# Kernel tuning notes

Hardware: AMD Instinct MI355X
Metric: run time of the kernel (lower is better)

## Reference

```python
import jax, jax.numpy as jnp
import numpy as np

B, S, D, NL = 512, 200, 128, 2
N_ITEMS = 50001
DH = 2 * D
DFF = 4 * D


def layer_norm(x, g, b, eps=1e-5):
    mu = x.mean(-1, keepdims=True)
    v = ((x - mu) ** 2).mean(-1, keepdims=True)
    return (x - mu) / jnp.sqrt(v + eps) * g + b


def lru_scan(h, lamb0, mask):
    # h: (B, L, DH) complex64, lamb0: (DH,) complex64, mask: (B, L) bool
    Bb, L, Dh = h.shape
    log2_L = int(np.ceil(np.log2(L)))
    lamb = lamb0.reshape(1, Dh)
    for i in range(1, log2_L + 1):
        l = 2 ** i
        h = h.reshape(Bb * L // l, l, Dh)
        m = mask.reshape(Bb * L // l, l)
        h1, h2 = h[:, : l // 2], h[:, l // 2:]
        if i > 1:
            lamb = jnp.concatenate([lamb, lamb * lamb[-1]], axis=0)  # powers lambda^1..lambda^(l/2)
        carry_gate = m[:, l // 2 - 1 : l // 2, None].astype(h.dtype)
        h2 = h2 + lamb * h1[:, -1:] * carry_gate
        h = jnp.concatenate([h1, h2], axis=1)
    return h.reshape(Bb, L, Dh)


def _forward(token_emb, emb_ln_g, emb_ln_b, params_log,
             in_wr, in_wi, in_br, in_bi, out_wr, out_wi, out_br, out_bi,
             lru_ln_g, lru_ln_b, w1, b1, w2, b2, ffn_ln_g, ffn_ln_b,
             item_seq, item_seq_len):
    mask = item_seq > 0                      # (B, S)
    x = token_emb[item_seq]                  # (B, S, D)
    x = layer_norm(x, emb_ln_g, emb_ln_b)
    seq_len = item_seq.shape[1]
    L = 2 ** int(np.ceil(np.log2(seq_len)))
    pad = L - seq_len
    x = jnp.pad(x, ((0, 0), (pad, 0), (0, 0)))        # left-pad seq to power of 2
    m = jnp.pad(mask, ((0, 0), (pad, 0)))
    n_layers = params_log.shape[0]
    for li in range(n_layers):
        pl = jnp.exp(params_log[li])                  # (3, DH): nu, theta, gamma
        nu, theta, gamma = pl[0], pl[1], pl[2]
        lamb0 = jnp.exp(jax.lax.complex(-nu, theta))  # (DH,)
        in_w = jax.lax.complex(in_wr[li], in_wi[li])
        in_b = jax.lax.complex(in_br[li], in_bi[li])
        h = (jnp.einsum('bld,hd->blh', x.astype(jnp.complex64), in_w) + in_b) * gamma
        h = lru_scan(h, lamb0, m)
        out_w = jax.lax.complex(out_wr[li], out_wi[li])
        out_b = jax.lax.complex(out_br[li], out_bi[li])
        y = (jnp.einsum('blh,dh->bld', h, out_w) + out_b).real + x
        x = layer_norm(y, lru_ln_g[li], lru_ln_b[li])
        # positionwise FFN with residual + post-LN
        hff = jax.nn.gelu(jnp.einsum('bld,fd->blf', x, w1[li]) + b1[li], approximate=False)
        x = layer_norm(jnp.einsum('blf,df->bld', hff, w2[li]) + b2[li] + x,
                       ffn_ln_g[li], ffn_ln_b[li])
    x = x[:, -seq_len:]                               # (B, S, D)
    idx = item_seq_len - 1
    return x[jnp.arange(x.shape[0]), idx]             # (B, D)


def setup_inputs() -> dict:
    key = jax.random.key(0)
    ks = jax.random.split(key, 24)
    std = 0.02
    item_seq = jax.random.randint(ks[0], (B, S), 0, N_ITEMS)
    item_seq_len = jax.random.randint(ks[1], (B,), 1, S + 1)
    # LRU diagonal init (matches torch init)
    r_min, r_max = 0.8, 0.99
    u1 = jax.random.uniform(ks[2], (NL, DH))
    u2 = jax.random.uniform(ks[3], (NL, DH))
    nu_log = jnp.log(-0.5 * jnp.log(u1 * (r_max ** 2 - r_min ** 2) + r_min ** 2))
    theta_log = jnp.log(u2 * 2.0 * np.pi)
    gamma_log = 0.5 * jnp.log(1.0 - jnp.exp(-2.0 * jnp.exp(nu_log)))
    params_log = jnp.stack([nu_log, theta_log, gamma_log], axis=1)  # (NL, 3, DH)
    rn = lambda k, sh: jax.random.normal(k, sh, dtype=jnp.float32) * std
    return {
        'token_emb': rn(ks[4], (N_ITEMS, D)),
        'emb_ln_g': jnp.ones((D,), jnp.float32), 'emb_ln_b': jnp.zeros((D,), jnp.float32),
        'params_log': params_log,
        'in_wr': rn(ks[5], (NL, DH, D)), 'in_wi': rn(ks[6], (NL, DH, D)),
        'in_br': rn(ks[7], (NL, DH)), 'in_bi': rn(ks[8], (NL, DH)),
        'out_wr': rn(ks[9], (NL, D, DH)), 'out_wi': rn(ks[10], (NL, D, DH)),
        'out_br': rn(ks[11], (NL, D)), 'out_bi': rn(ks[12], (NL, D)),
        'lru_ln_g': jnp.ones((NL, D), jnp.float32), 'lru_ln_b': jnp.zeros((NL, D), jnp.float32),
        'w1': rn(ks[13], (NL, DFF, D)), 'b1': rn(ks[14], (NL, DFF)),
        'w2': rn(ks[15], (NL, D, DFF)), 'b2': rn(ks[16], (NL, D)),
        'ffn_ln_g': jnp.ones((NL, D), jnp.float32), 'ffn_ln_b': jnp.zeros((NL, D), jnp.float32),
        'item_seq': item_seq, 'item_seq_len': item_seq_len,
    }


def reference(token_emb, emb_ln_g, emb_ln_b, params_log,
              in_wr, in_wi, in_br, in_bi, out_wr, out_wi, out_br, out_bi,
              lru_ln_g, lru_ln_b, w1, b1, w2, b2, ffn_ln_g, ffn_ln_b,
              item_seq, item_seq_len):
    return _forward(token_emb, emb_ln_g, emb_ln_b, params_log,
                    in_wr, in_wi, in_br, in_bi, out_wr, out_wi, out_br, out_bi,
                    lru_ln_g, lru_ln_b, w1, b1, w2, b2, ffn_ln_g, ffn_ln_b,
                    item_seq, item_seq_len)
```

## Files before the change

kernel.cpp:

```cpp
#include <hip/hip_runtime.h>
#include <hip/hip_bf16.h>
#include <math.h>

#define B_TOT 512
#define SEQ   200
#define D     128
#define DH    256
#define DFF   512
#define LPAD  256
#define PADL  56
#define NLAY  2
#define CST   260

typedef __attribute__((ext_vector_type(8))) short bf16x8;
typedef __attribute__((ext_vector_type(4))) float floatx4;

static __device__ inline float bf2f(ushort u) {
    union { unsigned int i; float f; } v; v.i = ((unsigned int)u) << 16; return v.f;
}
static __device__ inline ushort f2bf(float x) {
    union { float f; unsigned int i; } v; v.f = x;
    unsigned int r = (v.i + 0x7FFFu + ((v.i >> 16) & 1u)) >> 16;
    return (ushort)r;
}
static __device__ inline unsigned int pkbf(float a, float b) {
    union { __hip_bfloat162 h; unsigned int u; } v;
    v.h = __float22bfloat162_rn(make_float2(a, b));
    return v.u;
}
static __device__ inline void gld_lds16(const void* g, void* l) {
    __builtin_amdgcn_global_load_lds(
        (const __attribute__((address_space(1))) unsigned int*)g,
        (__attribute__((address_space(3))) unsigned int*)l, 16, 0, 0);
}

static __device__ inline size_t haddr(int b, int s, int k) {
    int p  = k >> 8;
    int ch = k & 255;
    int g  = ch >> 5;
    int cl = ch & 31;
    return (((((size_t)b * 8 + g) * 2 + p) * SEQ + s) * 32 + cl);
}

__global__ void setup_all_kernel(const float* __restrict__ params_log,
                                 const float* __restrict__ in_br,
                                 const float* __restrict__ in_bi,
                                 const float* __restrict__ in_wr,
                                 const float* __restrict__ in_wi,
                                 const float* __restrict__ out_wr,
                                 const float* __restrict__ out_wi,
                                 const float* __restrict__ w1,
                                 const float* __restrict__ w2,
                                 ushort* __restrict__ Winb,
                                 ushort* __restrict__ W2effb,
                                 ushort* __restrict__ w1b,
                                 ushort* __restrict__ w2b,
                                 float* __restrict__ lam_pow,
                                 float* __restrict__ scale_in,
                                 float* __restrict__ bias_in)
{
    int idx = blockIdx.x * blockDim.x + threadIdx.x;
    int li = idx >> 16;
    int e  = idx & 65535;

    {
        int gp = e >> 12, rem = e & 4095;
        int q = rem >> 3, e8 = rem & 7;
        int r = q >> 4, cs = q & 15;
        int c16 = cs ^ (r & 7);
        int n = (r < 16) ? (gp * 16 + r) : (256 + gp * 16 + (r - 16));
        int d = c16 * 8 + e8;
        float wv = (n < DH) ? in_wr[((size_t)li * DH + n) * D + d]
                            : in_wi[((size_t)li * DH + (n - DH)) * D + d];
        Winb[idx] = f2bf(wv);
    }
    {
        int k0c = e >> 13, rem = e & 8191;
        int q = rem >> 3, e8 = rem & 7;
        int r = q >> 3, cs = q & 7;
        int c16 = cs ^ (r & 7);
        int k = k0c * 64 + c16 * 8 + e8;
        float w2v = (k < DH) ? out_wr[((size_t)li * D + r) * DH + k]
                             : -out_wi[((size_t)li * D + r) * DH + (k - DH)];
        W2effb[idx] = f2bf(w2v);
    }
    {
        int row = e >> 7, col = e & 127;
        int ffc = row >> 7, rl = row & 127;
        int c16 = col >> 3, e8 = col & 7;
        int cs = c16 ^ (rl & 7);
        w1b[li * 65536 + ffc * 16384 + rl * 128 + cs * 8 + e8] = f2bf(w1[idx]);
    }
    {
        int dd2 = e >> 9, kk = e & 511;
        int ffc = kk >> 7, klc = kk & 127;
        int c16 = klc >> 3, e8 = klc & 7;
        int cs = c16 ^ (dd2 & 7);
        w2b[li * 65536 + ffc * 16384 + dd2 * 128 + cs * 8 + e8] = f2bf(w2[idx]);
    }

    if (blockIdx.x < NLAY) {
        int pli = blockIdx.x;
        int c = threadIdx.x;
        const float* pl = params_log + (size_t)pli * 3 * DH;
        float nu = expf(pl[c]);
        float th = expf(pl[DH + c]);
        float ga = expf(pl[2 * DH + c]);
        float mag = expf(-nu);
        float lr = mag * cosf(th);
        float lim = mag * sinf(th);
        float2* lp = (float2*)(lam_pow + (size_t)pli * 65536) + (size_t)c * 128;
        float pr = lr, pi = lim;
        lp[0] = make_float2(pr, pi);
        for (int k = 1; k < 128; ++k) {
            float nr = pr * lr - pi * lim;
            float ni = pr * lim + pi * lr;
            pr = nr; pi = ni;
            lp[k] = make_float2(pr, pi);
        }
        scale_in[pli * 2 * DH + c]      = ga;
        scale_in[pli * 2 * DH + DH + c] = ga;
        bias_in[pli * 2 * DH + c]       = in_br[pli * DH + c] * ga;
        bias_in[pli * 2 * DH + DH + c]  = in_bi[pli * DH + c] * ga;
    }
}

__global__ __launch_bounds__(512) void build_rowmap_kernel(
    const int* __restrict__ lenp, int Bc,
    int* __restrict__ total, int* __restrict__ rowmap)
{
    __shared__ int pre[513];
    int tid = threadIdx.x;
    int lv = (tid < Bc) ? lenp[tid] : 0;
    pre[tid + 1] = lv;
    if (tid == 0) pre[0] = 0;
    __syncthreads();
    for (int ofs = 1; ofs < 512; ofs <<= 1) {
        int v = pre[tid + 1];
        int vv = (tid + 1 > ofs) ? pre[tid + 1 - ofs] : 0;
        __syncthreads();
        pre[tid + 1] = v + vv;
        __syncthreads();
    }
    if (tid == 0) total[0] = pre[Bc];
    if (tid < Bc) {
        int base = pre[tid];
        int n = lv;
        int rb = tid * SEQ;
        for (int s = 0; s < n; ++s) rowmap[base + s] = rb + s;
    }
}

__global__ __launch_bounds__(256) void embed_ln_kernel(
    const float* __restrict__ emb, const int* __restrict__ seq,
    const int* __restrict__ lenp,
    const float* __restrict__ g, const float* __restrict__ bt,
    ushort* __restrict__ x)
{
    int row  = blockIdx.x * 4 + (threadIdx.x >> 6);
    int lane = threadIdx.x & 63;
    int b = row / SEQ, s = row - b * SEQ;
    if (s >= lenp[b]) return;
    int item = seq[row];
    float2 v = *(const float2*)(emb + (size_t)item * D + lane * 2);
    float ssum = v.x + v.y;
#pragma unroll
    for (int o = 32; o > 0; o >>= 1) ssum += __shfl_xor(ssum, o);
    float mu = ssum * (1.0f / D);
    float d0 = v.x - mu, d1 = v.y - mu;
    float vs = d0 * d0 + d1 * d1;
#pragma unroll
    for (int o = 32; o > 0; o >>= 1) vs += __shfl_xor(vs, o);
    float rstd = rsqrtf(vs * (1.0f / D) + 1e-5f);
    float2 gg = *(const float2*)(g + lane * 2);
    float2 bb = *(const float2*)(bt + lane * 2);
    unsigned int o2 = pkbf(d0 * rstd * gg.x + bb.x, d1 * rstd * gg.y + bb.y);
    *(unsigned int*)(x + (size_t)row * D + lane * 2) = o2;
}

template <bool LAST>
__global__ __launch_bounds__(512) void inproj_scan_kernel(
    const ushort* __restrict__ X, const ushort* __restrict__ Win,
    ushort* __restrict__ H, const float2* __restrict__ lamT,
    const int* __restrict__ seq, const int* __restrict__ lenp,
    const float* __restrict__ scale_in, const float* __restrict__ bias_in)
{
    __shared__ __align__(16) char smem[36864];
    __shared__ __align__(16) float mkf[LPAD];
    char*  Wsm = smem;
    char*  xs  = smem + 8192;
    float* stR = (float*)smem;
    float* stI = stR + 16 * CST;

    int gp = blockIdx.x, b = blockIdx.y;
    int tid = threadIdx.x;
    int l = tid & 63, w = tid >> 6;
    int ct = w & 1;
    int rq = w >> 1;
    int lr = l & 15, lq = l >> 4;
    int wbase = tid & ~63;

    int c  = tid >> 5;
    int tl = tid & 31;
    int t0 = tl * 8;
    int lbase = l & 32;

    int s_b = lenp[b] - 1;
    int tile_max = s_b >> 4;
    int nrows = (tile_max + 1) * 16;
    int tb = s_b + PADL;
    bool activeT = (t0 <= tb);

    const ushort* xrow = X + (size_t)b * SEQ * 128;
    gld_lds16(Win + (size_t)gp * 4096 + (size_t)tid * 8,
              Wsm + (size_t)wbase * 16);
    int nrA = nrows < 112 ? nrows : 112;
#pragma unroll
    for (int it = 0; it < 4; ++it) {
        int rbase = it * 32 + w * 4;
        int r = rbase + lq;
        int cs = lr ^ (r & 7);
        if (r < nrA)
            gld_lds16(xrow + (size_t)r * 128 + cs * 8, xs + rbase * 256);
    }

    const float2* myl = lamT + (size_t)(gp * 16 + c) * 128;

    if (tid < LPAD) {
        int t = tid;
        float m = 0.f;
        if (t >= PADL) m = (seq[(size_t)b * SEQ + (t - PADL)] > 0) ? 1.f : 0.f;
        mkf[t] = m;
    }
    __syncthreads();

    bf16x8 wf[4];
#pragma unroll
    for (int kk = 0; kk < 4; ++kk) {
        int ca = kk * 4 + lq;
        int wr = ct * 16 + lr;
        wf[kk] = *(const bf16x8*)(Wsm + wr * 256 + ((ca ^ (wr & 7)) * 16));
    }
    int tstart = rq ? (3 * rq + 1) : 0;
    int tcnt   = rq ? 3 : 4;
    floatx4 acc[4];
#pragma unroll
    for (int tt = 0; tt < 4; ++tt) acc[tt] = (floatx4)0.f;

    if (rq < 2) {
#pragma unroll
        for (int tt = 0; tt < 4; ++tt) {
            if (tt < tcnt && (tstart + tt) <= tile_max) {
                int t  = tstart + tt;
                int ar = t * 16 + lr;
#pragma unroll
                for (int kk = 0; kk < 4; ++kk) {
                    int ca = kk * 4 + lq;
                    bf16x8 af = *(const bf16x8*)(xs + ar * 256 + ((ca ^ (ar & 7)) * 16));
                    acc[tt] = __builtin_amdgcn_mfma_f32_16x16x32_bf16(wf[kk], af, acc[tt], 0, 0, 0);
                }
            }
        }
    }
    __syncthreads();

    if (nrows > 112) {
        int nrB = nrows < 200 ? nrows : 200;
#pragma unroll
        for (int it = 0; it < 3; ++it) {
            int rbase = it * 32 + w * 4;
            int rl_ = rbase + lq;
            int gr = 112 + rl_;
            int cs = lr ^ (rl_ & 7);
            if (gr < nrB)
                gld_lds16(xrow + (size_t)gr * 128 + cs * 8, xs + rbase * 256);
        }
    }
    __syncthreads();

    if (rq >= 2) {
#pragma unroll
        for (int tt = 0; tt < 4; ++tt) {
            if (tt < tcnt && (tstart + tt) <= tile_max) {
                int t  = tstart + tt;
                int ar = (t - 7) * 16 + lr;
#pragma unroll
                for (int kk = 0; kk < 4; ++kk) {
                    int ca = kk * 4 + lq;
                    bf16x8 af = *(const bf16x8*)(xs + ar * 256 + ((ca ^ (ar & 7)) * 16));
                    acc[tt] = __builtin_amdgcn_mfma_f32_16x16x32_bf16(wf[kk], af, acc[tt], 0, 0, 0);
                }
            }
        }
    }
    __syncthreads();

    float2 l14[4];
#pragma unroll
    for (int k = 0; k < 4; ++k) l14[k] = myl[k];
    float2 myl9 = myl[8];
    float2 lam_e[3];
#pragma unroll
    for (int i = 0; i < 3; ++i) {
        int half = 32 << i;
        int off = t0 & ((half << 1) - 1);
        int e = off - half;
        lam_e[i] = myl[e < 0 ? 0 : e];
    }
    float2 l7;
    l7.x = l14[3].x * l14[2].x - l14[3].y * l14[2].y;
    l7.y = l14[3].x * l14[2].y + l14[3].y * l14[2].x;

    {
        int zc = tid & 15, zk = tid >> 4;
        stR[zc * CST + zk] = 0.f; stI[zc * CST + zk] = 0.f;
        if (zk < PADL - 32) {
            stR[zc * CST + zk + 32] = 0.f; stI[zc * CST + zk + 32] = 0.f;
        }
    }
    {
        float4 g4 = *(const float4*)(scale_in + ct * 256 + gp * 16 + lq * 4);
        float4 b4 = *(const float4*)(bias_in  + ct * 256 + gp * 16 + lq * 4);
        float* dst = ct ? stI : stR;
#pragma unroll
        for (int tt = 0; tt < 4; ++tt) {
            if (tt < tcnt && (tstart + tt) <= tile_max) {
                int t = tstart + tt;
                int s = t * 16 + lr;
                if (s <= s_b) {
                    int pos = s + PADL;
                    dst[(lq * 4 + 0) * CST + pos] = acc[tt][0] * g4.x + b4.x;
                    dst[(lq * 4 + 1) * CST + pos] = acc[tt][1] * g4.y + b4.y;
                    dst[(lq * 4 + 2) * CST + pos] = acc[tt][2] * g4.z + b4.z;
                    dst[(lq * 4 + 3) * CST + pos] = acc[tt][3] * g4.w + b4.w;
                }
            }
        }
    }
    __syncthreads();

    __align__(16) float xr[8], xi[8], mf[8];
    *(floatx4*)&xr[0] = *(const floatx4*)(stR + c * CST + t0);
    *(floatx4*)&xr[4] = *(const floatx4*)(stR + c * CST + t0 + 4);
    *(floatx4*)&xi[0] = *(const floatx4*)(stI + c * CST + t0);
    *(floatx4*)&xi[4] = *(const floatx4*)(stI + c * CST + t0 + 4);
    *(floatx4*)&mf[0] = *(const floatx4*)(mkf + t0);
    *(floatx4*)&mf[4] = *(const floatx4*)(mkf + t0 + 4);

    if (activeT) {
#pragma unroll
        for (int k = 0; k < 8; k += 2) {
            float sr = xr[k] * mf[k], si = xi[k] * mf[k];
            xr[k+1] += l14[0].x * sr - l14[0].y * si;
            xi[k+1] += l14[0].x * si + l14[0].y * sr;
        }
#pragma unroll
        for (int k = 1; k < 8; k += 4) {
            float sr = xr[k] * mf[k], si = xi[k] * mf[k];
            xr[k+1] += l14[0].x * sr - l14[0].y * si;
            xi[k+1] += l14[0].x * si + l14[0].y * sr;
            xr[k+2] += l14[1].x * sr - l14[1].y * si;
            xi[k+2] += l14[1].x * si + l14[1].y * sr;
        }
        {
            float sr = xr[3] * mf[3], si = xi[3] * mf[3];
#pragma unroll
            for (int j = 0; j < 4; ++j) {
                xr[4+j] += l14[j].x * sr - l14[j].y * si;
                xi[4+j] += l14[j].x * si + l14[j].y * sr;
            }
        }
    } else {
        xr[7] = 0.f; xi[7] = 0.f;
    }

    float Ctr = 0.f, Cti = 0.f;
    float m7 = mf[7];
    float pxr = xr[7] * m7, pxi = xi[7] * m7;

#define TREE_LEVEL(SRC_TL, TGT, LE)                                          \
    {                                                                        \
        int srcl = lbase | (SRC_TL);                                         \
        float svx = __shfl(pxr, srcl);                                       \
        float svy = __shfl(pxi, srcl);                                       \
        if (activeT && (TGT)) {                                              \
            float2 le = (LE);                                                \
            float cr = le.x * svx - le.y * svy;                              \
            float ci = le.x * svy + le.y * svx;                              \
            Ctr += cr; Cti += ci;                                            \
            xr[7] += l7.x * cr - l7.y * ci;                                  \
            xi[7] += l7.x * ci + l7.y * cr;                                  \
            pxr = xr[7] * m7; pxi = xi[7] * m7;                              \
        }                                                                    \
    }

    TREE_LEVEL(tl & ~1,          tl & 1,  l14[0]);
    TREE_LEVEL((tl & ~3)  | 1,   tl & 2,  (tl & 1) ? myl9 : l14[0]);
    TREE_LEVEL((tl & ~7)  | 3,   tl & 4,  lam_e[0]);
    if (tb >= 64)  TREE_LEVEL((tl & ~15) | 7,  tl & 8,  lam_e[1]);
    if (tb >= 128) TREE_LEVEL((tl & ~31) | 15, tl & 16, lam_e[2]);
#undef TREE_LEVEL

    if (activeT && (!LAST || (unsigned)(tb - t0) < 7u)) {
        float2 l5, l6;
        l5.x = l14[3].x * l14[0].x - l14[3].y * l14[0].y;
        l5.y = l14[3].x * l14[0].y + l14[3].y * l14[0].x;
        l6.x = l14[3].x * l14[1].x - l14[3].y * l14[1].y;
        l6.y = l14[3].x * l14[1].y + l14[3].y * l14[1].x;
        xr[0] += Ctr;                               xi[0] += Cti;
        xr[1] += l14[0].x*Ctr - l14[0].y*Cti;       xi[1] += l14[0].x*Cti + l14[0].y*Ctr;
        xr[2] += l14[1].x*Ctr - l14[1].y*Cti;       xi[2] += l14[1].x*Cti + l14[1].y*Ctr;
        xr[3] += l14[2].x*Ctr - l14[2].y*Cti;       xi[3] += l14[2].x*Cti + l14[2].y*Ctr;
        xr[4] += l14[3].x*Ctr - l14[3].y*Cti;       xi[4] += l14[3].x*Cti + l14[3].y*Ctr;
        xr[5] += l5.x*Ctr - l5.y*Cti;               xi[5] += l5.x*Cti + l5.y*Ctr;
        xr[6] += l6.x*Ctr - l6.y*Cti;               xi[6] += l6.x*Cti + l6.y*Ctr;
    }

    if (LAST) {
        if (activeT && (unsigned)(tb - t0) < 8u) {
#pragma unroll
            for (int k = 0; k < 8; ++k)
                if (t0 + k == tb) {
                    stR[c * CST + tb] = xr[k];
                    stI[c * CST + tb] = xi[k];
                }
        }
    } else {
        if (activeT && tl >= 7) {
            *(floatx4*)(stR + c * CST + t0)     = *(const floatx4*)&xr[0];
            *(floatx4*)(stR + c * CST + t0 + 4) = *(const floatx4*)&xr[4];
            *(floatx4*)(stI + c * CST + t0)     = *(const floatx4*)&xi[0];
            *(floatx4*)(stI + c * CST + t0 + 4) = *(const floatx4*)&xi[4];
        }
    }
    __syncthreads();

    if (LAST) {
        if (tid < 32) {
            int p = tid >> 4, cc = tid & 15;
            float v = (p ? stI : stR)[cc * CST + tb];
            H[(size_t)b * 512 + p * 256 + gp * 16 + cc] = f2bf(v);
        }
    } else {
        int g  = gp >> 1;
        int hc = (gp & 1) * 16;
        ushort* baseg = H + (size_t)(b * 8 + g) * 2 * SEQ * 32 + hc;
#pragma unroll
        for (int it = 0; it < 4; ++it) {
            int idx4 = it * 512 + tid;
            if (idx4 < 2 * SEQ * 4) {
                int q  = idx4 & 3;
                int ps = idx4 >> 2;
                int p  = ps >= SEQ;
                int s  = ps - p * SEQ;
                if (s > s_b) continue;
                int t  = s + PADL;
                const float* sp = p ? stI : stR;
                float a0 = sp[(q * 4 + 0) * CST + t];
                float a1 = sp[(q * 4 + 1) * CST + t];
                float a2 = sp[(q * 4 + 2) * CST + t];
                float a3 = sp[(q * 4 + 3) * CST + t];
                uint2 raw;
                raw.x = pkbf(a0, a1);
                raw.y = pkbf(a2, a3);
                *(uint2*)(baseg + (size_t)ps * 32 + q * 4) = raw;
            }
        }
    }
}

__global__ __launch_bounds__(512) void outproj_kernel(
    const ushort* __restrict__ A, const ushort* __restrict__ Wimg,
    ushort* __restrict__ Cout,
    const int* __restrict__ rowmap, const int* __restrict__ totalp,
    const float* __restrict__ e0,
    const ushort* __restrict__ res,
    const float* __restrict__ lng, const float* __restrict__ lnb)
{
    int m0 = blockIdx.x * 256;
    int total = totalp[0];
    if (m0 >= total) return;
    __shared__ __align__(16) char As[32768];
    __shared__ __align__(16) char Bs[16384];
    __shared__ float2 lnS[2][256];
    int tid = threadIdx.x;
    int l = tid & 63, w = tid >> 6;
    int chh = w >> 2;
    int rh  = w & 3;
    int lr = l & 15, lq = l >> 4;
    int wbase = tid & ~63;

    int cst = tid & 7;
    int rr  = tid >> 3;
    int sb[4], ss[4];
#pragma unroll
    for (int it = 0; it < 4; ++it) {
        int gr = m0 + it * 64 + rr;
        if (gr >= total) gr = total - 1;
        int rm = rowmap[gr];
        sb[it] = rm / SEQ; ss[it] = rm - sb[it] * SEQ;
    }

    floatx4 acc[4][4];
#pragma unroll
    for (int i = 0; i < 4; ++i)
#pragma unroll
        for (int j = 0; j < 4; ++j) acc[i][j] = (floatx4)0.f;

    for (int k0c = 0; k0c < 8; ++k0c) {
        int k0 = k0c * 64;
        {
            const ushort* img = Wimg + (size_t)k0c * 8192;
#pragma unroll
            for (int it = 0; it < 2; ++it)
                gld_lds16(img + (size_t)(it * 512 + tid) * 8,
                          Bs + (size_t)(it * 512 + wbase) * 16);
        }
#pragma unroll
        for (int it = 0; it < 4; ++it) {
            int r = it * 64 + rr;
            uint4 va = *(const uint4*)(A + haddr(sb[it], ss[it], k0 + cst * 8));
            *(uint4*)(As + r * 128 + ((cst ^ (r & 7)) * 16)) = va;
        }
        __syncthreads();
#pragma unroll
        for (int kk = 0; kk < 2; ++kk) {
            bf16x8 wf[4], af[4];
            int ca = kk * 4 + lq;
#pragma unroll
            for (int i = 0; i < 4; ++i) {
                int rb = chh * 64 + i * 16 + lr;
                wf[i] = *(const bf16x8*)(Bs + rb * 128 + ((ca ^ (rb & 7)) * 16));
                int ra = rh * 64 + i * 16 + lr;
                af[i] = *(const bf16x8*)(As + ra * 128 + ((ca ^ (ra & 7)) * 16));
            }
#pragma unroll
            for (int i = 0; i < 4; ++i)
#pragma unroll
                for (int j = 0; j < 4; ++j)
                    acc[i][j] = __builtin_amdgcn_mfma_f32_16x16x32_bf16(
                        wf[i], af[j], acc[i][j], 0, 0, 0);
        }
        __syncthreads();
    }
// ... 119 lines not shown
                int ra = rh * 64 + i * 16 + lr;
                af[i] = *(const bf16x8*)(As + ra * 128 + ((ca ^ (ra & 7)) * 16));
            }
#pragma unroll
            for (int i = 0; i < 4; ++i)
#pragma unroll
                for (int j = 0; j < 4; ++j)
                    acc[i][j] = __builtin_amdgcn_mfma_f32_16x16x32_bf16(
                        wf[i], af[j], acc[i][j], 0, 0, 0);
        }
        __syncthreads();
    }

    int chb[4], arow[4];
#pragma unroll
    for (int i = 0; i < 4; ++i) chb[i] = chh * 64 + i * 16 + lq * 4;
#pragma unroll
    for (int j = 0; j < 4; ++j) arow[j] = m0 + rh * 64 + j * 16 + lr;

    {
        float4 bias[4], gv[4], bv[4];
#pragma unroll
        for (int i = 0; i < 4; ++i) {
            bias[i] = *(const float4*)(e0 + chb[i]);
            gv[i]   = *(const float4*)(lng + chb[i]);
            bv[i]   = *(const float4*)(lnb + chb[i]);
        }
#pragma unroll
        for (int j = 0; j < 4; ++j) {
            int br = arow[j] < Bc ? arow[j] : Bc - 1;
            int sb_ = lenp[br] - 1;
            const ushort* rbase = Xres + ((size_t)br * SEQ + sb_) * 128;
#pragma unroll
            for (int i = 0; i < 4; ++i) {
                ushort4 r4 = *(const ushort4*)(rbase + chb[i]);
                acc[i][j][0] += ((const float*)&bias[i])[0] + bf2f(r4.x);
                acc[i][j][1] += ((const float*)&bias[i])[1] + bf2f(r4.y);
                acc[i][j][2] += ((const float*)&bias[i])[2] + bf2f(r4.z);
                acc[i][j][3] += ((const float*)&bias[i])[3] + bf2f(r4.w);
            }
        }
#pragma unroll
        for (int j = 0; j < 4; ++j) {
            float s = 0.f, q = 0.f;
#pragma unroll
            for (int i = 0; i < 4; ++i)
#pragma unroll
                for (int reg = 0; reg < 4; ++reg) {
                    float v = acc[i][j][reg];
                    s += v; q += v * v;
                }
            s += __shfl_xor(s, 16); q += __shfl_xor(q, 16);
            s += __shfl_xor(s, 32); q += __shfl_xor(q, 32);
            if (lq == 0) lnS[chh][rh * 64 + j * 16 + lr] = make_float2(s, q);
        }
        __syncthreads();
#pragma unroll
        for (int j = 0; j < 4; ++j) {
            int rl = rh * 64 + j * 16 + lr;
            float2 s0 = lnS[0][rl], s1 = lnS[1][rl];
            float mu  = (s0.x + s1.x) * (1.0f / 128.0f);
            float var = (s0.y + s1.y) * (1.0f / 128.0f) - mu * mu;
            float rstd = rsqrtf(var + 1e-5f);
            if (arow[j] < Bc) {
#pragma unroll
                for (int i = 0; i < 4; ++i) {
                    uint2 u;
                    u.x = pkbf((acc[i][j][0] - mu) * rstd * ((const float*)&gv[i])[0] + ((const float*)&bv[i])[0],
                               (acc[i][j][1] - mu) * rstd * ((const float*)&gv[i])[1] + ((const float*)&bv[i])[1]);
                    u.y = pkbf((acc[i][j][2] - mu) * rstd * ((const float*)&gv[i])[2] + ((const float*)&bv[i])[2],
                               (acc[i][j][3] - mu) * rstd * ((const float*)&gv[i])[3] + ((const float*)&bv[i])[3]);
                    *(uint2*)(xc + (size_t)arow[j] * 128 + chb[i]) = u;
                }
            }
        }
    }
}

__global__ __launch_bounds__(256) void ffn_fused_kernel(
    ushort* __restrict__ X, const ushort* __restrict__ W1,
    const ushort* __restrict__ W2,
    const float* __restrict__ b1, const float* __restrict__ b2,
    const float* __restrict__ lng, const float* __restrict__ lnb,
    int Mtot, const int* __restrict__ rowmap, const int* __restrict__ totalp)
{
    int m0 = blockIdx.x * 64;
    int total = totalp ? totalp[0] : Mtot;
    if (m0 >= total) return;
    __shared__ __align__(16) char Bs[32768];
    __shared__ ushort Ps[64 * 136];
    __shared__ float2 lnS[2][64];
    int tid = threadIdx.x;
    int l = tid & 63, w = tid >> 6;
    int chh = w >> 1, rh = w & 1;
    int lr = l & 15, lq = l >> 4;
    int wbase = tid & ~63;

    int arow[2], rmrow[2];
#pragma unroll
    for (int j = 0; j < 2; ++j) {
        arow[j] = m0 + rh * 32 + j * 16 + lr;
        int rc = arow[j] < total ? arow[j] : total - 1;
        rmrow[j] = rowmap ? rowmap[rc] : rc;
    }

    bf16x8 af_x[8];
#pragma unroll
    for (int j = 0; j < 2; ++j)
#pragma unroll
        for (int kk2 = 0; kk2 < 4; ++kk2) {
            int k = kk2 * 32 + lq * 8;
            af_x[(j << 2) | kk2] = *(const bf16x8*)(X + (size_t)rmrow[j] * 128 + k);
        }

    floatx4 acc2[4][2];
#pragma unroll
    for (int i = 0; i < 4; ++i)
#pragma unroll
        for (int j = 0; j < 2; ++j) acc2[i][j] = (floatx4)0.f;

    for (int ffc = 0; ffc < 4; ++ffc) {
        if (ffc) __syncthreads();
        {
            const ushort* img = W1 + (size_t)ffc * 16384;
#pragma unroll
            for (int it = 0; it < 8; ++it)
                gld_lds16(img + (size_t)(it * 256 + tid) * 8,
                          Bs + (size_t)(it * 256 + wbase) * 16);
        }
        __syncthreads();

        floatx4 acc1[4][2];
#pragma unroll
        for (int i = 0; i < 4; ++i)
#pragma unroll
            for (int j = 0; j < 2; ++j) acc1[i][j] = (floatx4)0.f;
#pragma unroll
        for (int kk2 = 0; kk2 < 4; ++kk2) {
            int ca = kk2 * 4 + lq;
            bf16x8 wf[4];
#pragma unroll
            for (int i = 0; i < 4; ++i) {
                int rb = chh * 64 + i * 16 + lr;
                wf[i] = *(const bf16x8*)(Bs + rb * 256 + ((ca ^ (rb & 7)) * 16));
            }
#pragma unroll
            for (int i = 0; i < 4; ++i)
#pragma unroll
                for (int j = 0; j < 2; ++j)
                    acc1[i][j] = __builtin_amdgcn_mfma_f32_16x16x32_bf16(
                        wf[i], af_x[(j << 2) | kk2], acc1[i][j], 0, 0, 0);
        }

#pragma unroll
        for (int j = 0; j < 2; ++j) {
            int rowl = rh * 32 + j * 16 + lr;
#pragma unroll
            for (int i = 0; i < 4; ++i) {
                int ch0 = chh * 64 + i * 16 + lq * 4;
                float4 bv = *(const float4*)(b1 + ffc * 128 + ch0);
                float g0, g1, g2, g3, v;
                v = acc1[i][j][0] + bv.x; g0 = 0.5f * v * (1.0f + erff(v * 0.70710678118654752f));
                v = acc1[i][j][1] + bv.y; g1 = 0.5f * v * (1.0f + erff(v * 0.70710678118654752f));
                v = acc1[i][j][2] + bv.z; g2 = 0.5f * v * (1.0f + erff(v * 0.70710678118654752f));
                v = acc1[i][j][3] + bv.w; g3 = 0.5f * v * (1.0f + erff(v * 0.70710678118654752f));
                uint2 u; u.x = pkbf(g0, g1); u.y = pkbf(g2, g3);
                *(uint2*)(Ps + rowl * 136 + ch0) = u;
            }
        }
        __syncthreads();

        {
            const ushort* img = W2 + (size_t)ffc * 16384;
#pragma unroll
            for (int it = 0; it < 8; ++it)
                gld_lds16(img + (size_t)(it * 256 + tid) * 8,
                          Bs + (size_t)(it * 256 + wbase) * 16);
        }
        __syncthreads();

#pragma unroll
        for (int kk2 = 0; kk2 < 4; ++kk2) {
            int ca = kk2 * 4 + lq;
            bf16x8 wf[4], af[2];
#pragma unroll
            for (int i = 0; i < 4; ++i) {
                int rb = chh * 64 + i * 16 + lr;
                wf[i] = *(const bf16x8*)(Bs + rb * 256 + ((ca ^ (rb & 7)) * 16));
            }
#pragma unroll
            for (int j = 0; j < 2; ++j) {
                int rowl = rh * 32 + j * 16 + lr;
                af[j] = *(const bf16x8*)(Ps + rowl * 136 + kk2 * 32 + lq * 8);
            }
#pragma unroll
            for (int i = 0; i < 4; ++i)
#pragma unroll
                for (int j = 0; j < 2; ++j)
                    acc2[i][j] = __builtin_amdgcn_mfma_f32_16x16x32_bf16(
                        wf[i], af[j], acc2[i][j], 0, 0, 0);
        }
    }

    int chb[4];
#pragma unroll
    for (int i = 0; i < 4; ++i) chb[i] = chh * 64 + i * 16 + lq * 4;

    float4 bias[4], gv[4], bv[4];
#pragma unroll
    for (int i = 0; i < 4; ++i) {
        bias[i] = *(const float4*)(b2 + chb[i]);
        gv[i]   = *(const float4*)(lng + chb[i]);
        bv[i]   = *(const float4*)(lnb + chb[i]);
    }
#pragma unroll
    for (int j = 0; j < 2; ++j) {
#pragma unroll
        for (int i = 0; i < 4; ++i) {
            ushort4 r4 = *(const ushort4*)(X + (size_t)rmrow[j] * 128 + chb[i]);
            acc2[i][j][0] += ((const float*)&bias[i])[0] + bf2f(r4.x);
            acc2[i][j][1] += ((const float*)&bias[i])[1] + bf2f(r4.y);
            acc2[i][j][2] += ((const float*)&bias[i])[2] + bf2f(r4.z);
            acc2[i][j][3] += ((const float*)&bias[i])[3] + bf2f(r4.w);
        }
    }
#pragma unroll
    for (int j = 0; j < 2; ++j) {
        float s = 0.f, q = 0.f;
#pragma unroll
        for (int i = 0; i < 4; ++i)
#pragma unroll
            for (int reg = 0; reg < 4; ++reg) {
                float v = acc2[i][j][reg];
                s += v; q += v * v;
            }
        s += __shfl_xor(s, 16); q += __shfl_xor(q, 16);
        s += __shfl_xor(s, 32); q += __shfl_xor(q, 32);
        if (lq == 0) lnS[chh][rh * 32 + j * 16 + lr] = make_float2(s, q);
    }
    __syncthreads();
#pragma unroll
    for (int j = 0; j < 2; ++j) {
        int rl = rh * 32 + j * 16 + lr;
        float2 s0 = lnS[0][rl], s1 = lnS[1][rl];
        float mu  = (s0.x + s1.x) * (1.0f / 128.0f);
        float var = (s0.y + s1.y) * (1.0f / 128.0f) - mu * mu;
        float rstd = rsqrtf(var + 1e-5f);
        if (arow[j] < total) {
#pragma unroll
            for (int i = 0; i < 4; ++i) {
                uint2 u;
                u.x = pkbf((acc2[i][j][0] - mu) * rstd * ((const float*)&gv[i])[0] + ((const float*)&bv[i])[0],
                           (acc2[i][j][1] - mu) * rstd * ((const float*)&gv[i])[1] + ((const float*)&bv[i])[1]);
                u.y = pkbf((acc2[i][j][2] - mu) * rstd * ((const float*)&gv[i])[2] + ((const float*)&bv[i])[2],
                           (acc2[i][j][3] - mu) * rstd * ((const float*)&gv[i])[3] + ((const float*)&bv[i])[3]);
                *(uint2*)(X + (size_t)rmrow[j] * 128 + chb[i]) = u;
            }
        }
    }
}

__global__ void gather_final_kernel(const ushort* __restrict__ xc,
                                    float* __restrict__ out, int b0, int Bc)
{
    int i = blockIdx.x * 256 + threadIdx.x;
    if (i >= Bc * D) return;
    out[(size_t)b0 * D + i] = bf2f(xc[i]);
}

extern "C" void kernel_launch(void* const* d_in, const int* in_sizes, int n_in,
                              void* d_out, int out_size, void* d_ws, size_t ws_size,
                              hipStream_t stream)
{
    const float* token_emb  = (const float*)d_in[0];
    const float* emb_ln_g   = (const float*)d_in[1];
    const float* emb_ln_b   = (const float*)d_in[2];
    const float* params_log = (const float*)d_in[3];
    const float* in_wr      = (const float*)d_in[4];
    const float* in_wi      = (const float*)d_in[5];
    const float* in_br      = (const float*)d_in[6];
    const float* in_bi      = (const float*)d_in[7];
    const float* out_wr     = (const float*)d_in[8];
    const float* out_wi     = (const float*)d_in[9];
    const float* out_br     = (const float*)d_in[10];
    const float* lru_ln_g   = (const float*)d_in[12];
    const float* lru_ln_b   = (const float*)d_in[13];
    const float* w1         = (const float*)d_in[14];
    const float* b1         = (const float*)d_in[15];
    const float* w2         = (const float*)d_in[16];
    const float* b2         = (const float*)d_in[17];
    const float* ffn_ln_g   = (const float*)d_in[18];
    const float* ffn_ln_b   = (const float*)d_in[19];
    const int*   item_seq   = (const int*)d_in[20];
    const int*   item_seq_len = (const int*)d_in[21];
    float* out = (float*)d_out;

    char* ws = (char*)d_ws;
    ushort* Winb   = (ushort*)ws;                      ws += NLAY * 65536 * 2;
    ushort* W2effb = (ushort*)ws;                      ws += NLAY * 65536 * 2;
    ushort* w1b    = (ushort*)ws;                      ws += NLAY * 65536 * 2;
    ushort* w2b    = (ushort*)ws;                      ws += NLAY * 65536 * 2;
    float* lam_pow = (float*)ws;                       ws += NLAY * 65536 * 4;
    float* scale_in = (float*)ws;                      ws += NLAY * 512 * 4;
    float* bias_in  = (float*)ws;                      ws += NLAY * 512 * 4;
    size_t table_bytes = (size_t)(ws - (char*)d_ws);

    int Bc = B_TOT;
    while (Bc > 32) {
        size_t need = table_bytes
                    + (size_t)Bc * SEQ * (D * 2 + 2 * DH * 2)
                    + (size_t)(Bc * SEQ + 8) * 4 + 1024;
        if (need <= ws_size) break;
        Bc >>= 1;
    }
    ushort* xb = (ushort*)ws;                          ws += (size_t)Bc * SEQ * D * 2;
    ushort* hb = (ushort*)ws;                          ws += (size_t)Bc * SEQ * 2 * DH * 2;
    int* totalp = (int*)ws;                            ws += 8 * 4;
    int* rowmap = (int*)ws;
    ushort* Hc = hb;
    ushort* xc = hb + (size_t)Bc * 512;

    setup_all_kernel<<<NLAY * 65536 / 256, 256, 0, stream>>>(
        params_log, in_br, in_bi, in_wr, in_wi, out_wr, out_wi, w1, w2,
        Winb, W2effb, w1b, w2b, lam_pow, scale_in, bias_in);

    for (int b0 = 0; b0 < B_TOT; b0 += Bc) {
        int M = Bc * SEQ;
        const int* lenp = item_seq_len + b0;
        build_rowmap_kernel<<<1, 512, 0, stream>>>(lenp, Bc, totalp, rowmap);
        embed_ln_kernel<<<M / 4, 256, 0, stream>>>(
            token_emb, item_seq + (size_t)b0 * SEQ, lenp,
            emb_ln_g, emb_ln_b, xb);

        for (int li = 0; li < NLAY; ++li) {
            if (li < NLAY - 1) {
                inproj_scan_kernel<false><<<dim3(16, Bc), 512, 0, stream>>>(
                    xb, Winb + (size_t)li * 65536, hb,
                    (const float2*)(lam_pow + (size_t)li * 65536),
                    item_seq + (size_t)b0 * SEQ, lenp,
                    scale_in + li * 512, bias_in + li * 512);
                outproj_kernel<<<dim3(M / 256), 512, 0, stream>>>(
                    hb, W2effb + (size_t)li * 65536, xb, rowmap, totalp,
                    out_br + li * D, xb,
                    lru_ln_g + li * D, lru_ln_b + li * D);
                ffn_fused_kernel<<<dim3(M / 64), 256, 0, stream>>>(
                    xb, w1b + (size_t)li * 65536, w2b + (size_t)li * 65536,
                    b1 + li * DFF, b2 + li * D,
                    ffn_ln_g + li * D, ffn_ln_b + li * D, M, rowmap, totalp);
            } else {
                inproj_scan_kernel<true><<<dim3(16, Bc), 512, 0, stream>>>(
                    xb, Winb + (size_t)li * 65536, Hc,
                    (const float2*)(lam_pow + (size_t)li * 65536),
                    item_seq + (size_t)b0 * SEQ, lenp,
                    scale_in + li * 512, bias_in + li * 512);
                outproj_last_kernel<<<dim3((Bc + 255) / 256), 512, 0, stream>>>(
                    Hc, W2effb + (size_t)li * 65536, xc, Bc,
                    out_br + li * D, xb, lenp,
                    lru_ln_g + li * D, lru_ln_b + li * D);
                ffn_fused_kernel<<<dim3((Bc + 63) / 64), 256, 0, stream>>>(
                    xc, w1b + (size_t)li * 65536, w2b + (size_t)li * 65536,
                    b1 + li * DFF, b2 + li * D,
                    ffn_ln_g + li * D, ffn_ln_b + li * D, Bc,
                    (const int*)0, (const int*)0);
            }
        }
        gather_final_kernel<<<(Bc * D + 255) / 256, 256, 0, stream>>>(
            xc, out, b0, Bc);
    }
}
```

Before: 396.3 us.

## Fuse rowmap build into embed kernel, fold final gather, restrip scan LDS layout

The separate rowmap prefix-sum kernel is folded into the last block of the embedding layernorm kernel, and the final bf16-to-fp32 gather kernel is removed by having the last FFN kernel write fp32 output directly. This removes two launches per batch chunk. The scan stage's LDS staging changes from a channel-major padded layout to a time-strip layout with packed float2 math, aiming to cut bank conflicts and use packed FMA. The cost is more complex indexing and a single extra block doing serial rowmap writes.

Measured after the change: 386.0 us. -2.6%, faster.

```diff
diff --git a/kernel.cpp b/kernel.cpp
--- a/kernel.cpp
+++ b/kernel.cpp
@@ -10,10 +10,11 @@
 #define LPAD  256
 #define PADL  56
 #define NLAY  2
-#define CST   260
+#define SSTRIP 140
 
 typedef __attribute__((ext_vector_type(8))) short bf16x8;
 typedef __attribute__((ext_vector_type(4))) float floatx4;
+typedef __attribute__((ext_vector_type(2))) float floatx2;
 
 static __device__ inline float bf2f(ushort u) {
     union { unsigned int i; float f; } v; v.i = ((unsigned int)u) << 16; return v.f;
@@ -125,38 +126,37 @@
     }
 }
 
-__global__ __launch_bounds__(512) void build_rowmap_kernel(
-    const int* __restrict__ lenp, int Bc,
-    int* __restrict__ total, int* __restrict__ rowmap)
-{
-    __shared__ int pre[513];
-    int tid = threadIdx.x;
-    int lv = (tid < Bc) ? lenp[tid] : 0;
-    pre[tid + 1] = lv;
-    if (tid == 0) pre[0] = 0;
-    __syncthreads();
-    for (int ofs = 1; ofs < 512; ofs <<= 1) {
-        int v = pre[tid + 1];
-        int vv = (tid + 1 > ofs) ? pre[tid + 1 - ofs] : 0;
-        __syncthreads();
-        pre[tid + 1] = v + vv;
-        __syncthreads();
-    }
-    if (tid == 0) total[0] = pre[Bc];
-    if (tid < Bc) {
-        int base = pre[tid];
-        int n = lv;
-        int rb = tid * SEQ;
-        for (int s = 0; s < n; ++s) rowmap[base + s] = rb + s;
-    }
-}
-
 __global__ __launch_bounds__(256) void embed_ln_kernel(
     const float* __restrict__ emb, const int* __restrict__ seq,
     const int* __restrict__ lenp,
     const float* __restrict__ g, const float* __restrict__ bt,
-    ushort* __restrict__ x)
+    ushort* __restrict__ x,
+    int Bc, int* __restrict__ total, int* __restrict__ rowmap)
 {
+    if (blockIdx.x == gridDim.x - 1) {
+        __shared__ int ps[257];
+        int t = threadIdx.x;
+        int b0_ = 2 * t, b1_ = 2 * t + 1;
+        int lv0 = (b0_ < Bc) ? lenp[b0_] : 0;
+        int lv1 = (b1_ < Bc) ? lenp[b1_] : 0;
+        ps[t + 1] = lv0 + lv1;
+        if (t == 0) ps[0] = 0;
+        __syncthreads();
+        for (int ofs = 1; ofs < 256; ofs <<= 1) {
+            int v = ps[t + 1];
+            int vv = (t + 1 > ofs) ? ps[t + 1 - ofs] : 0;
+            __syncthreads();
+            ps[t + 1] = v + vv;
+            __syncthreads();
+        }
+        if (t == 255) total[0] = ps[256];
+        int base = ps[t];
+        int rb0 = b0_ * SEQ, rb1 = b1_ * SEQ;
+        for (int s = 0; s < lv0; ++s) rowmap[base + s] = rb0 + s;
+        base += lv0;
+        for (int s = 0; s < lv1; ++s) rowmap[base + s] = rb1 + s;
+        return;
+    }
     int row  = blockIdx.x * 4 + (threadIdx.x >> 6);
     int lane = threadIdx.x & 63;
     int b = row / SEQ, s = row - b * SEQ;
@@ -186,11 +186,11 @@
     const float* __restrict__ scale_in, const float* __restrict__ bias_in)
 {
     __shared__ __align__(16) char smem[36864];
-    __shared__ __align__(16) float mkf[LPAD];
+    __shared__ __align__(16) float mkfS[32 * 12];
     char*  Wsm = smem;
     char*  xs  = smem + 8192;
-    float* stR = (float*)smem;
-    float* stI = stR + 16 * CST;
+    float* stR2 = (float*)smem;
+    float* stI2 = stR2 + 32 * SSTRIP;
 
     int gp = blockIdx.x, b = blockIdx.y;
     int tid = threadIdx.x;
@@ -204,6 +204,7 @@
     int tl = tid & 31;
     int t0 = tl * 8;
     int lbase = l & 32;
+    int coff = (c >> 2) * 36 + (c & 3) * 8;
 
     int s_b = lenp[b] - 1;
     int tile_max = s_b >> 4;
@@ -230,7 +231,7 @@
         int t = tid;
         float m = 0.f;
         if (t >= PADL) m = (seq[(size_t)b * SEQ + (t - PADL)] > 0) ? 1.f : 0.f;
-        mkf[t] = m;
+        mkfS[(t >> 3) * 12 + (t & 7)] = m;
     }
     __syncthreads();
 
@@ -311,72 +312,82 @@
     l7.x = l14[3].x * l14[2].x - l14[3].y * l14[2].y;
     l7.y = l14[3].x * l14[2].y + l14[3].y * l14[2].x;
 
-    {
-        int zc = tid & 15, zk = tid >> 4;
-        stR[zc * CST + zk] = 0.f; stI[zc * CST + zk] = 0.f;
-        if (zk < PADL - 32) {
-            stR[zc * CST + zk + 32] = 0.f; stI[zc * CST + zk + 32] = 0.f;
-        }
-    }
+    for (int idx = tid; idx < 7 * SSTRIP; idx += 512) { stR2[idx] = 0.f; stI2[idx] = 0.f; }
     {
         float4 g4 = *(const float4*)(scale_in + ct * 256 + gp * 16 + lq * 4);
         float4 b4 = *(const float4*)(bias_in  + ct * 256 + gp * 16 + lq * 4);
-        float* dst = ct ? stI : stR;
+        float* base = ct ? stI2 : stR2;
 #pragma unroll
         for (int tt = 0; tt < 4; ++tt) {
             if (tt < tcnt && (tstart + tt) <= tile_max) {
                 int t = tstart + tt;
                 int s = t * 16 + lr;
                 if (s <= s_b) {
-                    int pos = s + PADL;
-                    dst[(lq * 4 + 0) * CST + pos] = acc[tt][0] * g4.x + b4.x;
-                    dst[(lq * 4 + 1) * CST + pos] = acc[tt][1] * g4.y + b4.y;
-                    dst[(lq * 4 + 2) * CST + pos] = acc[tt][2] * g4.z + b4.z;
-                    dst[(lq * 4 + 3) * CST + pos] = acc[tt][3] * g4.w + b4.w;
+                    float* dst = base + (2 * t + 7 + (lr >> 3)) * SSTRIP
+                               + lq * 36 + (lr & 7);
+                    dst[0]  = acc[tt][0] * g4.x + b4.x;
+                    dst[8]  = acc[tt][1] * g4.y + b4.y;
+                    dst[16] = acc[tt][2] * g4.z + b4.z;
+                    dst[24] = acc[tt][3] * g4.w + b4.w;
                 }
             }
         }
     }
     __syncthreads();
 
-    __align__(16) float xr[8], xi[8], mf[8];
-    *(floatx4*)&xr[0] = *(const floatx4*)(stR + c * CST + t0);
-    *(floatx4*)&xr[4] = *(const floatx4*)(stR + c * CST + t0 + 4);
-    *(floatx4*)&xi[0] = *(const floatx4*)(stI + c * CST + t0);
-    *(floatx4*)&xi[4] = *(const floatx4*)(stI + c * CST + t0 + 4);
-    *(floatx4*)&mf[0] = *(const floatx4*)(mkf + t0);
-    *(floatx4*)&mf[4] = *(const floatx4*)(mkf + t0 + 4);
+    floatx2 Xr[4], Xi[4], Mf[4];
+    {
+        const float* pr = stR2 + tl * SSTRIP + coff;
+        const float* pi = stI2 + tl * SSTRIP + coff;
+        floatx4 r0 = *(const floatx4*)pr;
+        floatx4 r1 = *(const floatx4*)(pr + 4);
+        floatx4 i0 = *(const floatx4*)pi;
+        floatx4 i1 = *(const floatx4*)(pi + 4);
+        floatx4 m0 = *(const floatx4*)(mkfS + tl * 12);
+        floatx4 m1 = *(const floatx4*)(mkfS + tl * 12 + 4);
+        Xr[0] = floatx2{r0[0], r0[1]}; Xr[1] = floatx2{r0[2], r0[3]};
+        Xr[2] = floatx2{r1[0], r1[1]}; Xr[3] = floatx2{r1[2], r1[3]};
+        Xi[0] = floatx2{i0[0], i0[1]}; Xi[1] = floatx2{i0[2], i0[3]};
+        Xi[2] = floatx2{i1[0], i1[1]}; Xi[3] = floatx2{i1[2], i1[3]};
+        Mf[0] = floatx2{m0[0], m0[1]}; Mf[1] = floatx2{m0[2], m0[3]};
+        Mf[2] = floatx2{m1[0], m1[1]}; Mf[3] = floatx2{m1[2], m1[3]};
+    }
+
+    float l0x = l14[0].x, l0y = l14[0].y;
+    floatx2 L01R = floatx2{l14[0].x, l14[1].x};
+    floatx2 L01I = floatx2{l14[0].y, l14[1].y};
+    floatx2 L23R = floatx2{l14[2].x, l14[3].x};
+    floatx2 L23I = floatx2{l14[2].y, l14[3].y};
 
     if (activeT) {
 #pragma unroll
-        for (int k = 0; k < 8; k += 2) {
-            float sr = xr[k] * mf[k], si = xi[k] * mf[k];
-            xr[k+1] += l14[0].x * sr - l14[0].y * si;
-            xi[k+1] += l14[0].x * si + l14[0].y * sr;
-        }
-#pragma unroll
-        for (int k = 1; k < 8; k += 4) {
-            float sr = xr[k] * mf[k], si = xi[k] * mf[k];
-            xr[k+1] += l14[0].x * sr - l14[0].y * si;
-            xi[k+1] += l14[0].x * si + l14[0].y * sr;
-            xr[k+2] += l14[1].x * sr - l14[1].y * si;
-            xi[k+2] += l14[1].x * si + l14[1].y * sr;
+        for (int p = 0; p < 4; ++p) {
+            float sr = Xr[p].x * Mf[p].x, si = Xi[p].x * Mf[p].x;
+            Xr[p].y += l0x * sr; Xr[p].y -= l0y * si;
+            Xi[p].y += l0x * si; Xi[p].y += l0y * sr;
+        }
+#pragma unroll
+        for (int p = 0; p < 2; ++p) {
+            int sp_ = p * 2;
+            float sr = Xr[sp_].y * Mf[sp_].y, si = Xi[sp_].y * Mf[sp_].y;
+            Xr[sp_ + 1] += sr * L01R; Xr[sp_ + 1] -= si * L01I;
+            Xi[sp_ + 1] += si * L01R; Xi[sp_ + 1] += sr * L01I;
         }
         {
-            float sr = xr[3] * mf[3], si = xi[3] * mf[3];
-#pragma unroll
-            for (int j = 0; j < 4; ++j) {
-                xr[4+j] += l14[j].x * sr - l14[j].y * si;
-                xi[4+j] += l14[j].x * si + l14[j].y * sr;
-            }
-        }
-    } else {
-        xr[7] = 0.f; xi[7] = 0.f;
-    }
-
+            float sr = Xr[1].y * Mf[1].y, si = Xi[1].y * Mf[1].y;
+            Xr[2] += sr * L01R; Xr[2] -= si * L01I;
+            Xi[2] += si * L01R; Xi[2] += sr * L01I;
+            Xr[3] += sr * L23R; Xr[3] -= si * L23I;
+            Xi[3] += si * L23R; Xi[3] += sr * L23I;
+        }
+    }
+
+    float x7r, x7i;
+    if (activeT) { x7r = Xr[3].y; x7i = Xi[3].y; }
+    else         { x7r = 0.f;     x7i = 0.f; }
     float Ctr = 0.f, Cti = 0.f;
-    float m7 = mf[7];
-    float pxr = xr[7] * m7, pxi = xi[7] * m7;
+    float m7 = Mf[3].y;
+    float pxr = x7r * m7, pxi = x7i * m7;
 
 #define TREE_LEVEL(SRC_TL, TGT, LE)                                          \
     {                                                                        \
@@ -388,9 +399,9 @@
             float cr = le.x * svx - le.y * svy;                              \
             float ci = le.x * svy + le.y * svx;                              \
             Ctr += cr; Cti += ci;                                            \
-            xr[7] += l7.x * cr - l7.y * ci;                                  \
-            xi[7] += l7.x * ci + l7.y * cr;                                  \
-            pxr = xr[7] * m7; pxi = xi[7] * m7;                              \
+            x7r += l7.x * cr - l7.y * ci;                                    \
+            x7i += l7.x * ci + l7.y * cr;                                    \
+            pxr = x7r * m7; pxi = x7i * m7;                                  \
         }                                                                    \
     }
 
@@ -407,30 +418,43 @@
         l5.y = l14[3].x * l14[0].y + l14[3].y * l14[0].x;
         l6.x = l14[3].x * l14[1].x - l14[3].y * l14[1].y;
         l6.y = l14[3].x * l14[1].y + l14[3].y * l14[1].x;
-        xr[0] += Ctr;                               xi[0] += Cti;
-        xr[1] += l14[0].x*Ctr - l14[0].y*Cti;       xi[1] += l14[0].x*Cti + l14[0].y*Ctr;
-        xr[2] += l14[1].x*Ctr - l14[1].y*Cti;       xi[2] += l14[1].x*Cti + l14[1].y*Ctr;
-        xr[3] += l14[2].x*Ctr - l14[2].y*Cti;       xi[3] += l14[2].x*Cti + l14[2].y*Ctr;
-        xr[4] += l14[3].x*Ctr - l14[3].y*Cti;       xi[4] += l14[3].x*Cti + l14[3].y*Ctr;
-        xr[5] += l5.x*Ctr - l5.y*Cti;               xi[5] += l5.x*Cti + l5.y*Ctr;
-        xr[6] += l6.x*Ctr - l6.y*Cti;               xi[6] += l6.x*Cti + l6.y*Ctr;
-    }
+        Xr[0].x += Ctr;                                 Xi[0].x += Cti;
+        Xr[0].y += l14[0].x * Ctr; Xr[0].y -= l14[0].y * Cti;
+        Xi[0].y += l14[0].x * Cti; Xi[0].y += l14[0].y * Ctr;
+        Xr[1].x += l14[1].x * Ctr; Xr[1].x -= l14[1].y * Cti;
+        Xi[1].x += l14[1].x * Cti; Xi[1].x += l14[1].y * Ctr;
+        Xr[1].y += l14[2].x * Ctr; Xr[1].y -= l14[2].y * Cti;
+        Xi[1].y += l14[2].x * Cti; Xi[1].y += l14[2].y * Ctr;
+        Xr[2].x += l14[3].x * Ctr; Xr[2].x -= l14[3].y * Cti;
+        Xi[2].x += l14[3].x * Cti; Xi[2].x += l14[3].y * Ctr;
+        Xr[2].y += l5.x * Ctr;     Xr[2].y -= l5.y * Cti;
+        Xi[2].y += l5.x * Cti;     Xi[2].y += l5.y * Ctr;
+        Xr[3].x += l6.x * Ctr;     Xr[3].x -= l6.y * Cti;
+        Xi[3].x += l6.x * Cti;     Xi[3].x += l6.y * Ctr;
+    }
+    Xr[3].y = x7r; Xi[3].y = x7i;
 
     if (LAST) {
         if (activeT && (unsigned)(tb - t0) < 8u) {
 #pragma unroll
             for (int k = 0; k < 8; ++k)
                 if (t0 + k == tb) {
-                    stR[c * CST + tb] = xr[k];
-                    stI[c * CST + tb] = xi[k];
+                    float vr = (k & 1) ? Xr[k >> 1].y : Xr[k >> 1].x;
+                    float vi = (k & 1) ? Xi[k >> 1].y : Xi[k >> 1].x;
+                    stR2[tl * SSTRIP + coff + k] = vr;
+                    stI2[tl * SSTRIP + coff + k] = vi;
                 }
         }
     } else {
         if (activeT && tl >= 7) {
-            *(floatx4*)(stR + c * CST + t0)     = *(const floatx4*)&xr[0];
-            *(floatx4*)(stR + c * CST + t0 + 4) = *(const floatx4*)&xr[4];
-            *(floatx4*)(stI + c * CST + t0)     = *(const floatx4*)&xi[0];
-            *(floatx4*)(stI + c * CST + t0 + 4) = *(const floatx4*)&xi[4];
+            floatx4 r0 = floatx4{Xr[0].x, Xr[0].y, Xr[1].x, Xr[1].y};
+            floatx4 r1 = floatx4{Xr[2].x, Xr[2].y, Xr[3].x, Xr[3].y};
+            floatx4 i0 = floatx4{Xi[0].x, Xi[0].y, Xi[1].x, Xi[1].y};
+            floatx4 i1 = floatx4{Xi[2].x, Xi[2].y, Xi[3].x, Xi[3].y};
+            *(floatx4*)(stR2 + tl * SSTRIP + coff)     = r0;
+            *(floatx4*)(stR2 + tl * SSTRIP + coff + 4) = r1;
+            *(floatx4*)(stI2 + tl * SSTRIP + coff)     = i0;
+            *(floatx4*)(stI2 + tl * SSTRIP + coff + 4) = i1;
         }
     }
     __syncthreads();
@@ -438,7 +462,8 @@
     if (LAST) {
         if (tid < 32) {
             int p = tid >> 4, cc = tid & 15;
-            float v = (p ? stI : stR)[cc * CST + tb];
+            int fi = (tb >> 3) * SSTRIP + (cc >> 2) * 36 + (cc & 3) * 8 + (tb & 7);
+            float v = (p ? stI2 : stR2)[fi];
             H[(size_t)b * 512 + p * 256 + gp * 16 + cc] = f2bf(v);
         }
     } else {
@@ -454,12 +479,9 @@
                 int p  = ps >= SEQ;
                 int s  = ps - p * SEQ;
                 if (s > s_b) continue;
-                int t  = s + PADL;
-                const float* sp = p ? stI : stR;
-                float a0 = sp[(q * 4 + 0) * CST + t];
-                float a1 = sp[(q * 4 + 1) * CST + t];
-                float a2 = sp[(q * 4 + 2) * CST + t];
-                float a3 = sp[(q * 4 + 3) * CST + t];
+                const float* sp = (p ? stI2 : stR2)
+                                + ((s + PADL) >> 3) * SSTRIP + q * 36 + (s & 7);
+                float a0 = sp[0], a1 = sp[8], a2 = sp[16], a3 = sp[24];
                 uint2 raw;
                 raw.x = pkbf(a0, a1);
                 raw.y = pkbf(a2, a3);
@@ -745,7 +767,8 @@
     const ushort* __restrict__ W2,
     const float* __restrict__ b1, const float* __restrict__ b2,
     const float* __restrict__ lng, const float* __restrict__ lnb,
-    int Mtot, const int* __restrict__ rowmap, const int* __restrict__ totalp)
+    int Mtot, const int* __restrict__ rowmap, const int* __restrict__ totalp,
+    float* __restrict__ outp, int b0f)
 {
     int m0 = blockIdx.x * 64;
     int total = totalp ? totalp[0] : Mtot;
@@ -910,25 +933,29 @@
         float var = (s0.y + s1.y) * (1.0f / 128.0f) - mu * mu;
         float rstd = rsqrtf(var + 1e-5f);
         if (arow[j] < total) {
-#pragma unroll
-            for (int i = 0; i < 4; ++i) {
-                uint2 u;
-                u.x = pkbf((acc2[i][j][0] - mu) * rstd * ((const float*)&gv[i])[0] + ((const float*)&bv[i])[0],
-                           (acc2[i][j][1] - mu) * rstd * ((const float*)&gv[i])[1] + ((const float*)&bv[i])[1]);
-                u.y = pkbf((acc2[i][j][2] - mu) * rstd * ((const float*)&gv[i])[2] + ((const float*)&bv[i])[2],
-                           (acc2[i][j][3] - mu) * rstd * ((const float*)&gv[i])[3] + ((const float*)&bv[i])[3]);
-                *(uint2*)(X + (size_t)rmrow[j] * 128 + chb[i]) = u;
-            }
-        }
-    }
-}
-
-__global__ void gather_final_kernel(const ushort* __restrict__ xc,
-                                    float* __restrict__ out, int b0, int Bc)
-{
-    int i = blockIdx.x * 256 + threadIdx.x;
-    if (i >= Bc * D) return;
-    out[(size_t)b0 * D + i] = bf2f(xc[i]);
+            if (outp) {
+#pragma unroll
+                for (int i = 0; i < 4; ++i) {
+                    float4 o;
+                    o.x = (acc2[i][j][0] - mu) * rstd * ((const float*)&gv[i])[0] + ((const float*)&bv[i])[0];
+                    o.y = (acc2[i][j][1] - mu) * rstd * ((const float*)&gv[i])[1] + ((const float*)&bv[i])[1];
+                    o.z = (acc2[i][j][2] - mu) * rstd * ((const float*)&gv[i])[2] + ((const float*)&bv[i])[2];
+                    o.w = (acc2[i][j][3] - mu) * rstd * ((const float*)&gv[i])[3] + ((const float*)&bv[i])[3];
+                    *(float4*)(outp + (size_t)(b0f + rmrow[j]) * 128 + chb[i]) = o;
+                }
+            } else {
+#pragma unroll
+                for (int i = 0; i < 4; ++i) {
+                    uint2 u;
+                    u.x = pkbf((acc2[i][j][0] - mu) * rstd * ((const float*)&gv[i])[0] + ((const float*)&bv[i])[0],
+                               (acc2[i][j][1] - mu) * rstd * ((const float*)&gv[i])[1] + ((const float*)&bv[i])[1]);
+                    u.y = pkbf((acc2[i][j][2] - mu) * rstd * ((const float*)&gv[i])[2] + ((const float*)&bv[i])[2],
+                               (acc2[i][j][3] - mu) * rstd * ((const float*)&gv[i])[3] + ((const float*)&bv[i])[3]);
+                    *(uint2*)(X + (size_t)rmrow[j] * 128 + chb[i]) = u;
+                }
+            }
+        }
+    }
 }
 
 extern "C" void kernel_launch(void* const* d_in, const int* in_sizes, int n_in,
@@ -990,10 +1017,9 @@
     for (int b0 = 0; b0 < B_TOT; b0 += Bc) {
         int M = Bc * SEQ;
         const int* lenp = item_seq_len + b0;
-        build_rowmap_kernel<<<1, 512, 0, stream>>>(lenp, Bc, totalp, rowmap);
-        embed_ln_kernel<<<M / 4, 256, 0, stream>>>(
+        embed_ln_kernel<<<M / 4 + 1, 256, 0, stream>>>(
             token_emb, item_seq + (size_t)b0 * SEQ, lenp,
-            emb_ln_g, emb_ln_b, xb);
+            emb_ln_g, emb_ln_b, xb, Bc, totalp, rowmap);
 
         for (int li = 0; li < NLAY; ++li) {
             if (li < NLAY - 1) {
@@ -1009,7 +1035,8 @@
                 ffn_fused_kernel<<<dim3(M / 64), 256, 0, stream>>>(
                     xb, w1b + (size_t)li * 65536, w2b + (size_t)li * 65536,
                     b1 + li * DFF, b2 + li * D,
-                    ffn_ln_g + li * D, ffn_ln_b + li * D, M, rowmap, totalp);
+                    ffn_ln_g + li * D, ffn_ln_b + li * D, M, rowmap, totalp,
+                    (float*)0, 0);
             } else {
                 inproj_scan_kernel<true><<<dim3(16, Bc), 512, 0, stream>>>(
                     xb, Winb + (size_t)li * 65536, Hc,
@@ -1024,10 +1051,8 @@
                     xc, w1b + (size_t)li * 65536, w2b + (size_t)li * 65536,
                     b1 + li * DFF, b2 + li * D,
                     ffn_ln_g + li * D, ffn_ln_b + li * D, Bc,
-                    (const int*)0, (const int*)0);
-            }
-        }
-        gather_final_kernel<<<(Bc * D + 255) / 256, 256, 0, stream>>>(
-            xc, out, b0, Bc);
-    }
-}
+                    (const int*)0, (const int*)0, out, b0);
+            }
+        }
+    }
+}
```
